# Kernel optimization log

Hardware: AMD Instinct MI355X
Metric: run time of the kernel (lower is better)

## Reference

```python
import jax, jax.numpy as jnp
import numpy as np

L, B, D = 1024, 32, 1024
USE_TANH = True  # use_tanh=1

def setup_inputs() -> dict:
    key = jax.random.key(0)
    k1, k2, k3, k4 = jax.random.split(key, 4)
    return {
        "x": jax.random.normal(k1, (L, B, D), jnp.float32),
        "c0": jax.random.normal(k2, (B, D), jnp.float32),
        "weight": jax.random.normal(k3, (D, D, 3), jnp.float32) * 0.02,
        "bias": jax.random.normal(k4, (2 * D,), jnp.float32) * 0.02,
    }

def reference(x, c0, weight, bias):
    # x: [L,B,D], weight: [D_in, D_out, 3], bias: [2*D_out], c0: [B,D_out]
    d = weight.shape[1]
    # u = x @ weight.view(n_in, 3*n_out) with per-output-dim interleaving -> [L,B,D,3]
    u = jnp.einsum('lbi,iok->lbok', x, weight)
    u0 = u[..., 0]                       # candidate
    f = jax.nn.sigmoid(u[..., 1] + bias[:d])    # forget gate
    r = jax.nn.sigmoid(u[..., 2] + bias[d:])    # highway/reset gate

    def step(c_prev, inp):
        f_t, u0_t = inp
        c_t = f_t * c_prev + (1.0 - f_t) * u0_t
        return c_t, c_t

    _, c = jax.lax.scan(step, c0, (f, u0))  # c: [L,B,D]
    g = jnp.tanh(c) if USE_TANH else c
    h = r * g + (1.0 - r) * x               # highway connection (n_in == n_out path)
    return h, c
```

## Files before the change

### kernel.cpp

```cpp
#include <hip/hip_runtime.h>
#include <hip/hip_bf16.h>
#include <stdint.h>

#define L_DIM 1024
#define B_DIM 32
#define D_DIM 1024
#define M_DIM (L_DIM * B_DIM)
#define N3_DIM (3 * D_DIM)
#define K_DIM D_DIM
#define LBD ((int64_t)L_DIM * B_DIM * D_DIM)
#define NBD (B_DIM * D_DIM)
#define NCHUNK 32
#define CLEN 32

#define BM 256
#define BN 256
#define BK 64
#define NMT (M_DIM / BM)
#define NNT (N3_DIM / BN)
#define NKT (K_DIM / BK)
#define NITER (NKT / 2)

typedef __bf16 bf16_t;
typedef bf16_t bf16x8 __attribute__((ext_vector_type(8)));
typedef float f32x4 __attribute__((ext_vector_type(4)));

__device__ __forceinline__ unsigned short f2bf(float f) {
    union { float f; unsigned u; } v; v.f = f;
    unsigned u = v.u;
    u += 0x7FFFu + ((u >> 16) & 1u);
    return (unsigned short)(u >> 16);
}
__device__ __forceinline__ float bf2f(unsigned short h) {
    union { unsigned u; float f; } v; v.u = ((unsigned)h) << 16;
    return v.f;
}

__global__ void cvt_x_kernel(const float* __restrict__ x, unsigned short* __restrict__ xb) {
    int64_t i0 = ((int64_t)blockIdx.x * blockDim.x + threadIdx.x) * 4;
    int64_t stride = (int64_t)gridDim.x * blockDim.x * 4;
    for (int64_t i = i0; i < LBD; i += stride) {
        float4 v = *reinterpret_cast<const float4*>(x + i);
        ushort4 o;
        o.x = f2bf(v.x); o.y = f2bf(v.y); o.z = f2bf(v.z); o.w = f2bf(v.w);
        *reinterpret_cast<ushort4*>(xb + i) = o;
    }
}

__global__ void cvt_w_kernel(const float* __restrict__ w, unsigned short* __restrict__ wT) {
    __shared__ float tile[64][65];
    int bid = blockIdx.x;
    int k  = bid >> 8;
    int o0 = ((bid >> 4) & 15) * 64;
    int i0 = (bid & 15) * 64;
    int t = threadIdx.x;
    {
        int o = t & 63, ib = t >> 6;
        #pragma unroll
        for (int it = 0; it < 16; ++it) {
            int i = ib + it * 4;
            tile[o][i] = w[((int64_t)(i0 + i) * 1024 + (o0 + o)) * 3 + k];
        }
    }
    __syncthreads();
    {
        int i = t & 63, ob = t >> 6;
        #pragma unroll
        for (int ot = 0; ot < 16; ++ot) {
            int o = ob + ot * 4;
            wT[(int64_t)(k * 1024 + o0 + o) * 1024 + (i0 + i)] = f2bf(tile[o][i]);
        }
    }
}

__device__ __forceinline__ void gload_lds16(const void* g, void* l) {
    __builtin_amdgcn_global_load_lds(
        (const __attribute__((address_space(1))) unsigned int*)g,
        (__attribute__((address_space(3))) unsigned int*)l,
        16, 0, 0);
}

#define BARRIER() do { asm volatile("" ::: "memory"); __builtin_amdgcn_s_barrier(); asm volatile("" ::: "memory"); } while (0)
#define WAIT_LGKM0() asm volatile("s_waitcnt lgkmcnt(0)" ::: "memory")
#define WAIT_LGKM8() asm volatile("s_waitcnt lgkmcnt(8)" ::: "memory")
#define VMCNT(n) asm volatile("s_waitcnt vmcnt(" #n ")" ::: "memory")

__global__ __launch_bounds__(512, 2) void gemm_kernel(
    const unsigned short* __restrict__ A,
    const unsigned short* __restrict__ Bt,
    const float* __restrict__ bias,
    float* __restrict__ u0_out,
    unsigned short* __restrict__ fb,
    unsigned short* __restrict__ rb)
{
    __shared__ __align__(16) unsigned short a_lds[2][2][128 * 64];
    __shared__ __align__(16) unsigned short b_lds[2][2][128 * 64];

    int bid = blockIdx.x;
    int swz = (bid & 7) * (NMT * NNT / 8) + (bid >> 3);
    int nt = swz % NNT, mt = swz / NNT;
    int m0 = mt * BM, n0 = nt * BN;

    int tid = threadIdx.x;
    int w = tid >> 6, lane = tid & 63;
    int wm = w >> 2, wn = w & 3;
    int l15 = lane & 15, l4 = lane >> 4;
    int pcx = l15 & 7;

    int srow = w * 8 + (lane >> 3);
    int scol = ((lane & 7) ^ ((lane >> 3) & 7)) << 3;
    const unsigned short* Asrc = A  + (int64_t)(m0 + srow) * K_DIM + scol;
    const unsigned short* Bsrc = Bt + (int64_t)(n0 + srow) * K_DIM + scol;
    unsigned short* dstA = &a_lds[0][0][0] + w * 8 * 64;
    unsigned short* dstB = &b_lds[0][0][0] + w * 8 * 64;

    auto stageA = [&](int buf, int half, int kt) {
        if (kt >= NKT) return;
        const unsigned short* s = Asrc + (int64_t)half * 128 * K_DIM + kt * BK;
        unsigned short* d = dstA + (buf * 2 + half) * (128 * 64);
        gload_lds16(s, d);
        gload_lds16(s + (int64_t)64 * K_DIM, d + 64 * 64);
    };
    auto stageB = [&](int buf, int half, int kt) {
        if (kt >= NKT) return;
        const unsigned short* s = Bsrc + (int64_t)half * 128 * K_DIM + kt * BK;
        unsigned short* d = dstB + (buf * 2 + half) * (128 * 64);
        gload_lds16(s, d);
        gload_lds16(s + (int64_t)64 * K_DIM, d + 64 * 64);
    };

    auto rdA_ = [&](int buf, int mh, int im, int ks) -> bf16x8 {
        int rr = wm * 64 + im * 16 + l15;
        int pc = ((ks * 4 + l4) ^ pcx) << 3;
        return *reinterpret_cast<const bf16x8*>(&a_lds[buf][mh][rr * 64 + pc]);
    };
    auto rdB_ = [&](int buf, int nh, int jn, int ks) -> bf16x8 {
        int rr = wn * 32 + jn * 16 + l15;
        int pc = ((ks * 4 + l4) ^ pcx) << 3;
        return *reinterpret_cast<const bf16x8*>(&b_lds[buf][nh][rr * 64 + pc]);
    };

    f32x4 acc[8][4];
    #pragma unroll
    for (int i = 0; i < 8; ++i)
        #pragma unroll
        for (int j = 0; j < 4; ++j) acc[i][j] = (f32x4){0.f, 0.f, 0.f, 0.f};

    bf16x8 af[4][2], b0[2][2], b1[2][2];

#define QUAD(MH, NH, BB)                                                            \
    do {                                                                            \
        __builtin_amdgcn_s_setprio(1);                                              \
        _Pragma("unroll")                                                           \
        for (int im = 0; im < 4; ++im)                                              \
            _Pragma("unroll")                                                       \
            for (int jn = 0; jn < 2; ++jn)                                          \
                _Pragma("unroll")                                                   \
                for (int ks = 0; ks < 2; ++ks)                                      \
                    acc[(MH)*4 + im][(NH)*2 + jn] =                                 \
                        __builtin_amdgcn_mfma_f32_16x16x32_bf16(                    \
                            af[im][ks], BB[jn][ks], acc[(MH)*4 + im][(NH)*2 + jn],  \
                            0, 0, 0);                                               \
        __builtin_amdgcn_s_setprio(0);                                              \
    } while (0)

    stageA(0, 0, 0);
    stageB(0, 0, 0);
    stageB(0, 1, 0);
    stageA(0, 1, 0);
    stageA(1, 0, 1);
    stageB(1, 0, 1);
    stageB(1, 1, 1);
    VMCNT(6);
    BARRIER();

    for (int t = 0; t < NITER; ++t) {
        int t2 = t * 2;
        #pragma unroll
        for (int im = 0; im < 4; ++im) { af[im][0] = rdA_(0, 0, im, 0); af[im][1] = rdA_(0, 0, im, 1); }
        #pragma unroll
        for (int jn = 0; jn < 2; ++jn) { b0[jn][0] = rdB_(0, 0, jn, 0); b0[jn][1] = rdB_(0, 0, jn, 1); }
        stageA(1, 1, t2 + 1);
        WAIT_LGKM8();
        BARRIER();
        WAIT_LGKM0();
        QUAD(0, 0, b0);
        BARRIER();
        #pragma unroll
        for (int jn = 0; jn < 2; ++jn) { b1[jn][0] = rdB_(0, 1, jn, 0); b1[jn][1] = rdB_(0, 1, jn, 1); }
        stageA(0, 0, t2 + 2);
        BARRIER();
        WAIT_LGKM0();
        QUAD(0, 1, b1);
        BARRIER();
        #pragma unroll
        for (int im = 0; im < 4; ++im) { af[im][0] = rdA_(0, 1, im, 0); af[im][1] = rdA_(0, 1, im, 1); }
        stageB(0, 0, t2 + 2);
        BARRIER();
        WAIT_LGKM0();
        QUAD(1, 0, b0);
        BARRIER();
        stageB(0, 1, t2 + 2);
        if (t < NITER - 1) { VMCNT(6); } else { VMCNT(0); }
        BARRIER();
        QUAD(1, 1, b1);
        BARRIER();
        #pragma unroll
        for (int im = 0; im < 4; ++im) { af[im][0] = rdA_(1, 0, im, 0); af[im][1] = rdA_(1, 0, im, 1); }
        #pragma unroll
        for (int jn = 0; jn < 2; ++jn) { b0[jn][0] = rdB_(1, 0, jn, 0); b0[jn][1] = rdB_(1, 0, jn, 1); }
        stageA(0, 1, t2 + 2);
        WAIT_LGKM8();
        BARRIER();
        WAIT_LGKM0();
        QUAD(0, 0, b0);
        BARRIER();
        #pragma unroll
        for (int jn = 0; jn < 2; ++jn) { b1[jn][0] = rdB_(1, 1, jn, 0); b1[jn][1] = rdB_(1, 1, jn, 1); }
        stageA(1, 0, t2 + 3);
        BARRIER();
        WAIT_LGKM0();
        QUAD(0, 1, b1);
        BARRIER();
        #pragma unroll
        for (int im = 0; im < 4; ++im) { af[im][0] = rdA_(1, 1, im, 0); af[im][1] = rdA_(1, 1, im, 1); }
        stageB(1, 0, t2 + 3);
        BARRIER();
        WAIT_LGKM0();
        QUAD(1, 0, b0);
        BARRIER();
        stageB(1, 1, t2 + 3);
        if (t < NITER - 1) { VMCNT(6); } else { VMCNT(0); }
        BARRIER();
        QUAD(1, 1, b1);
        BARRIER();
    }

    int region = n0 >> 10;
    #pragma unroll
    for (int i = 0; i < 8; ++i) {
        int mh = i >> 2, im = i & 3;
        #pragma unroll
        for (int j = 0; j < 4; ++j) {
            int nh = j >> 1, jn = j & 1;
            f32x4 v = acc[i][j];
            int row0 = m0 + mh * 128 + wm * 64 + im * 16 + l4 * 4;
            int col  = (n0 + nh * 128 + wn * 32 + jn * 16 + l15) & 1023;
            #pragma unroll
            for (int jj = 0; jj < 4; ++jj) {
                int64_t idx = (int64_t)(row0 + jj) * 1024 + col;
                float val = v[jj];
                if (region == 0) {
                    u0_out[idx] = val;
                } else if (region == 1) {
                    fb[idx] = f2bf(1.0f / (1.0f + __expf(-(val + bias[col]))));
                } else {
                    rb[idx] = f2bf(1.0f / (1.0f + __expf(-(val + bias[1024 + col]))));
                }
            }
        }
    }
#undef QUAD
}


__global__ void scan_phase1(const unsigned short* __restrict__ fb,
                            const float* __restrict__ u0_arr,
                            float* __restrict__ Aout, float* __restrict__ Bout) {
    int t = blockIdx.x * blockDim.x + threadIdx.x;
    int idx = t & (NBD - 1);
    int chunk = t >> 15;
    int64_t base = (int64_t)chunk * CLEN * NBD + idx;
    float Ap = 1.0f, Bv = 0.0f;
    #pragma unroll 8
    for (int i = 0; i < CLEN; ++i, base += NBD) {
        float f = bf2f(fb[base]);
        float u0 = u0_arr[base];
        Bv = u0 + f * (Bv - u0);
        Ap *= f;
    }
    Aout[t] = Ap; Bout[t] = Bv;
}

__global__ void scan_phase2(const float* __restrict__ c0, const float* __restrict__ Aarr,
                            const float* __restrict__ Barr, float* __restrict__ cin) {
    int idx = blockIdx.x * blockDim.x + threadIdx.x;
    float c = c0[idx];
    #pragma unroll
    for (int ch = 0; ch < NCHUNK; ++ch) {
        cin[ch * NBD + idx] = c;
        c = Aarr[ch * NBD + idx] * c + Barr[ch * NBD + idx];
    }
}

__global__ void scan_phase3(const float* __restrict__ x,
                            const unsigned short* __restrict__ fb,
                            const unsigned short* __restrict__ rb,
                            const float* __restrict__ cin,
                            float* __restrict__ out_h, float* __restrict__ out_c) {
    int t = blockIdx.x * blockDim.x + threadIdx.x;
    int idx = t & (NBD - 1);
    int chunk = t >> 15;
    float c = cin[t];
    int64_t base = (int64_t)chunk * CLEN * NBD + idx;
    #pragma unroll 4
    for (int i = 0; i < CLEN; ++i, base += NBD) {
        float f  = bf2f(fb[base]);
        float u0 = out_c[base];
        c = u0 + f * (c - u0);
        out_c[base] = c;
        float e = __expf(2.0f * c);
        float g = (e - 1.0f) / (e + 1.0f);
        float r = bf2f(rb[base]);
        float xv = x[base];
        out_h[base] = xv + r * (g - xv);
    }
}

extern "C" void kernel_launch(void* const* d_in, const int* in_sizes, int n_in,
                              void* d_out, int out_size, void* d_ws, size_t ws_size,
                              hipStream_t stream) {
    const float* x    = (const float*)d_in[0];
    const float* c0   = (const float*)d_in[1];
    const float* wgt  = (const float*)d_in[2];
    const float* bias = (const float*)d_in[3];
    float* out = (float*)d_out;

    unsigned short* xb = (unsigned short*)d_ws;
    unsigned short* wT = xb + (int64_t)M_DIM * K_DIM;
    unsigned short* fb = wT + (int64_t)N3_DIM * K_DIM;
    unsigned short* rb = fb + LBD;

    float* Aarr = (float*)d_ws;
    float* Barr = Aarr + NCHUNK * NBD;
    float* cin  = Barr + NCHUNK * NBD;

    cvt_x_kernel<<<8192, 256, 0, stream>>>(x, xb);
    cvt_w_kernel<<<768, 256, 0, stream>>>(wgt, wT);
    gemm_kernel<<<NMT * NNT, 512, 0, stream>>>(xb, wT, bias, out + LBD, fb, rb);
    scan_phase1<<<(NCHUNK * NBD) / 256, 256, 0, stream>>>(fb, out + LBD, Aarr, Barr);
    scan_phase2<<<NBD / 256, 256, 0, stream>>>(c0, Aarr, Barr, cin);
    scan_phase3<<<(NCHUNK * NBD) / 256, 256, 0, stream>>>(x, fb, rb, cin, out, out + LBD);
}
```

Before: 518.0 us.

## Software-pipeline LDS fragment reads under MFMA quads and halve barriers per stage

Restructures the GEMM main loop so the LDS fragment reads for the next quad are issued right after the current quad's MFMAs. Each quad now uses one barrier instead of two, and the global-load vmcnt wait threshold is tightened from 6 to 2. The aim is to hide LDS read latency behind matrix math and cut synchronisation overhead in the K loop. The risks are register pressure from holding extra fragments and correctness hazards from the reduced barriers and changed wait counts.

```diff
diff --git a/kernel.cpp b/kernel.cpp
--- a/kernel.cpp
+++ b/kernel.cpp
@@ -82,7 +82,6 @@
 
 #define BARRIER() do { asm volatile("" ::: "memory"); __builtin_amdgcn_s_barrier(); asm volatile("" ::: "memory"); } while (0)
 #define WAIT_LGKM0() asm volatile("s_waitcnt lgkmcnt(0)" ::: "memory")
-#define WAIT_LGKM8() asm volatile("s_waitcnt lgkmcnt(8)" ::: "memory")
 #define VMCNT(n) asm volatile("s_waitcnt vmcnt(" #n ")" ::: "memory")
 
 __global__ __launch_bounds__(512, 2) void gemm_kernel(
@@ -148,6 +147,22 @@
 
     bf16x8 af[4][2], b0[2][2], b1[2][2];
 
+#define RD_A(BUF, MH)                                                               \
+    do {                                                                            \
+        _Pragma("unroll")                                                           \
+        for (int im = 0; im < 4; ++im) {                                            \
+            af[im][0] = rdA_((BUF), (MH), im, 0);                                   \
+            af[im][1] = rdA_((BUF), (MH), im, 1);                                   \
+        }                                                                           \
+    } while (0)
+#define RD_B(DST, BUF, NH)                                                          \
+    do {                                                                            \
+        _Pragma("unroll")                                                           \
+        for (int jn = 0; jn < 2; ++jn) {                                            \
+            DST[jn][0] = rdB_((BUF), (NH), jn, 0);                                  \
+            DST[jn][1] = rdB_((BUF), (NH), jn, 1);                                  \
+        }                                                                           \
+    } while (0)
 #define QUAD(MH, NH, BB)                                                            \
     do {                                                                            \
         __builtin_amdgcn_s_setprio(1);                                              \
@@ -171,69 +186,54 @@
     stageA(1, 0, 1);
     stageB(1, 0, 1);
     stageB(1, 1, 1);
-    VMCNT(6);
+    VMCNT(2);
     BARRIER();
-
+    RD_A(0, 0);
+    RD_B(b0, 0, 0);
+
+    #pragma unroll 1
     for (int t = 0; t < NITER; ++t) {
         int t2 = t * 2;
-        #pragma unroll
-        for (int im = 0; im < 4; ++im) { af[im][0] = rdA_(0, 0, im, 0); af[im][1] = rdA_(0, 0, im, 1); }
-        #pragma unroll
-        for (int jn = 0; jn < 2; ++jn) { b0[jn][0] = rdB_(0, 0, jn, 0); b0[jn][1] = rdB_(0, 0, jn, 1); }
+        BARRIER();
+        WAIT_LGKM0();
+        RD_B(b1, 0, 1);
+        QUAD(0, 0, b0);
         stageA(1, 1, t2 + 1);
-        WAIT_LGKM8();
-        BARRIER();
-        WAIT_LGKM0();
+        BARRIER();
+        WAIT_LGKM0();
+        QUAD(0, 1, b1);
+        RD_A(0, 1);
+        stageA(0, 0, t2 + 2);
+        BARRIER();
+        WAIT_LGKM0();
+        QUAD(1, 0, b0);
+        RD_B(b0, 1, 0);
+        stageB(0, 0, t2 + 2);
+        BARRIER();
+        QUAD(1, 1, b1);
+        RD_A(1, 0);
+        stageB(0, 1, t2 + 2);
+        if (t < NITER - 1) { VMCNT(2); } else { VMCNT(0); }
+        BARRIER();
+        WAIT_LGKM0();
+        RD_B(b1, 1, 1);
         QUAD(0, 0, b0);
-        BARRIER();
-        #pragma unroll
-        for (int jn = 0; jn < 2; ++jn) { b1[jn][0] = rdB_(0, 1, jn, 0); b1[jn][1] = rdB_(0, 1, jn, 1); }
-        stageA(0, 0, t2 + 2);
+        stageA(0, 1, t2 + 2);
         BARRIER();
         WAIT_LGKM0();
         QUAD(0, 1, b1);
-        BARRIER();
-        #pragma unroll
-        for (int im = 0; im < 4; ++im) { af[im][0] = rdA_(0, 1, im, 0); af[im][1] = rdA_(0, 1, im, 1); }
-        stageB(0, 0, t2 + 2);
+        RD_A(1, 1);
+        stageA(1, 0, t2 + 3);
         BARRIER();
         WAIT_LGKM0();
         QUAD(1, 0, b0);
-        BARRIER();
-        stageB(0, 1, t2 + 2);
-        if (t < NITER - 1) { VMCNT(6); } else { VMCNT(0); }
+        RD_B(b0, 0, 0);
+        stageB(1, 0, t2 + 3);
         BARRIER();
         QUAD(1, 1, b1);
-        BARRIER();
-        #pragma unroll
-        for (int im = 0; im < 4; ++im) { af[im][0] = rdA_(1, 0, im, 0); af[im][1] = rdA_(1, 0, im, 1); }
-        #pragma unroll
-        for (int jn = 0; jn < 2; ++jn) { b0[jn][0] = rdB_(1, 0, jn, 0); b0[jn][1] = rdB_(1, 0, jn, 1); }
-        stageA(0, 1, t2 + 2);
-        WAIT_LGKM8();
-        BARRIER();
-        WAIT_LGKM0();
-        QUAD(0, 0, b0);
-        BARRIER();
-        #pragma unroll
-        for (int jn = 0; jn < 2; ++jn) { b1[jn][0] = rdB_(1, 1, jn, 0); b1[jn][1] = rdB_(1, 1, jn, 1); }
-        stageA(1, 0, t2 + 3);
-        BARRIER();
-        WAIT_LGKM0();
-        QUAD(0, 1, b1);
-        BARRIER();
-        #pragma unroll
-        for (int im = 0; im < 4; ++im) { af[im][0] = rdA_(1, 1, im, 0); af[im][1] = rdA_(1, 1, im, 1); }
-        stageB(1, 0, t2 + 3);
-        BARRIER();
-        WAIT_LGKM0();
-        QUAD(1, 0, b0);
-        BARRIER();
+        RD_A(0, 0);
         stageB(1, 1, t2 + 3);
-        if (t < NITER - 1) { VMCNT(6); } else { VMCNT(0); }
-        BARRIER();
-        QUAD(1, 1, b1);
-        BARRIER();
+        if (t < NITER - 1) { VMCNT(2); } else { VMCNT(0); }
     }
 
     int region = n0 >> 10;
@@ -260,6 +260,8 @@
             }
         }
     }
+#undef RD_A
+#undef RD_B
 #undef QUAD
 }
 
```

New measurement: 506.6 us. 2.2% less time.
